# Performance work log

Measured on AMD Instinct MI355X. Metric: run time of the kernel, lower is better.

The kernel has to match this reference:

```python
import jax, jax.numpy as jnp
import numpy as np

B, S, D, H = 2, 4096, 1024, 16
HD = D // H
KCONV = 4


def _rmsnorm(x, scale, eps=1e-6):
    return x * jax.lax.rsqrt(jnp.mean(x * x, axis=-1, keepdims=True) + eps) * scale


def _l2norm(x, eps=1e-6):
    return x * jax.lax.rsqrt(jnp.sum(x * x, axis=-1, keepdims=True) + eps)


def _causal_dwconv_silu(x, w):
    # x: [B,S,D], w: [D,K] depthwise taps (tap K-1 multiplies x[t])
    k = w.shape[1]
    s = x.shape[1]
    xp = jnp.pad(x, ((0, 0), (k - 1, 0), (0, 0)))
    out = sum(xp[:, i:i + s, :] * w[:, i] for i in range(k))
    return jax.nn.silu(out)


def _p20_scan(x, decay_log, theta):
    # BLOCK_DIAGONAL_2 rotary-state linear recurrence: channels paired into
    # complex state, s_t = a * s_{t-1} + u_t with a = exp(-exp(decay_log) + i*theta).
    b, s, d = x.shape
    xc = x.reshape(b, s, d // 2, 2)
    u = jax.lax.complex(xc[..., 0], xc[..., 1])  # [B,S,D/2]
    a = jnp.exp(-jnp.exp(decay_log)) * jnp.exp(1j * theta)  # [D/2] complex, |a|<1

    def step(carry, u_t):
        st = carry * a + u_t
        return st, st

    _, ys = jax.lax.scan(step, jnp.zeros((b, d // 2), u.dtype), jnp.swapaxes(u, 0, 1))
    ys = jnp.swapaxes(ys, 0, 1)  # [B,S,D/2]
    return jnp.stack([ys.real, ys.imag], axis=-1).reshape(b, s, d)


def _gated_delta_rule(q, k, v, g, beta):
    # q,k,v: [B,S,H,Dh]; g,beta: [B,S,H]. State S: [B,H,K,V].
    scale = q.shape[-1] ** -0.5
    q = _l2norm(q)
    k = _l2norm(k)
    qt, kt, vt = (jnp.moveaxis(t, 1, 0) for t in (q, k, v))
    gt, bt = (jnp.moveaxis(t, 1, 0) for t in (g, beta))
    s0 = jnp.zeros((q.shape[0], q.shape[2], q.shape[3], v.shape[3]), v.dtype)

    def step(state, inp):
        q_t, k_t, v_t, g_t, b_t = inp
        state = state * jnp.exp(g_t)[..., None, None]
        v_err = (v_t - jnp.einsum('bhkv,bhk->bhv', state, k_t)) * b_t[..., None]
        state = state + jnp.einsum('bhk,bhv->bhkv', k_t, v_err)
        o_t = jnp.einsum('bhkv,bhk->bhv', state, q_t) * scale
        return state, o_t

    _, o = jax.lax.scan(step, s0, (qt, kt, vt, gt, bt))
    return jnp.moveaxis(o, 0, 1)  # [B,S,H,V]


def setup_inputs() -> dict:
    key = jax.random.key(0)
    ks = jax.random.split(key, 16)
    w = lambda k, shp, s=0.02: (jax.random.normal(k, shp, jnp.float32) * s)
    ctrl_out = 3 * D + 2 * H + D  # q,k,v,decay,beta,output_gate
    ctrl_b = jnp.concatenate([
        jnp.zeros((3 * D,), jnp.float32),
        jnp.full((H,), 1.5, jnp.float32),       # decay bias
        jnp.full((H,), -2.0, jnp.float32),      # beta bias
        jnp.full((D,), -1.5, jnp.float32),      # output gate bias
    ])
    # depthwise conv init: delta at last tap + small noise
    def conv_w(k):
        base = jnp.zeros((D, KCONV), jnp.float32).at[:, -1].set(1.0)
        return base + w(k, (D, KCONV), 0.02)
    return {
        'hidden': jax.random.normal(ks[0], (B, S, D), jnp.float32),
        'p20_decay_log': w(ks[1], (D // 2,), 1.0),
        'p20_theta': jax.random.uniform(ks[2], (D // 2,), jnp.float32, 0.0, 2.0 * np.pi),
        'ctrl_W': w(ks[3], (D, ctrl_out)),
        'ctrl_b': ctrl_b,
        'p20c_W': w(ks[4], (D, 3 * D), 0.001),  # 0.05-scaled init
        'qconv_w': conv_w(ks[5]),
        'kconv_w': conv_w(ks[6]),
        'vconv_w': conv_w(ks[7]),
        'mnorm_scale': jnp.ones((HD,), jnp.float32),
        'vnorm_scale': jnp.ones((D,), jnp.float32),
        'ramp_logit': jnp.full((D,), -4.595, jnp.float32),  # logit(0.01)
        'out_W': w(ks[8], (2 * D, D), 0.02),
        'out_b': jnp.zeros((D,), jnp.float32),
    }


def reference(hidden, p20_decay_log, p20_theta, ctrl_W, ctrl_b, p20c_W,
              qconv_w, kconv_w, vconv_w, mnorm_scale, vnorm_scale,
              ramp_logit, out_W, out_b):
    b, s, d = hidden.shape
    # P20 vector-state side channel
    p20_read = _p20_scan(hidden, p20_decay_log, p20_theta)
    normed_p20 = _rmsnorm(p20_read, vnorm_scale)
    p20_q, p20_k, p20_v = jnp.split(normed_p20 @ p20c_W, 3, axis=-1)
    ramp = jax.nn.sigmoid(ramp_logit)  # [D]
    # packed control projection
    ctrl = hidden @ ctrl_W + ctrl_b
    q_in, k_in, v_in, dec_in, beta_in, gate_in = jnp.split(
        ctrl, np.cumsum([d, d, d, H, H]).tolist(), axis=-1)
    # causal depthwise conv + SiLU
    q_in = _causal_dwconv_silu(q_in, qconv_w)
    k_in = _causal_dwconv_silu(k_in, kconv_w)
    v_in = _causal_dwconv_silu(v_in, vconv_w)
    # P20-conditioned heads
    queries = (q_in + ramp * p20_q).reshape(b, s, H, HD)
    keys = (k_in + ramp * p20_k).reshape(b, s, H, HD)
    values = (v_in + ramp * p20_v).reshape(b, s, H, HD)
    g = jax.nn.log_sigmoid(dec_in.astype(jnp.float32)).astype(hidden.dtype)  # [B,S,H]
    beta = jax.nn.sigmoid(beta_in)
    reads = _gated_delta_rule(queries, keys, values, g, beta)
    normed_reads = _rmsnorm(reads, mnorm_scale).reshape(b, s, d)
    fused = jnp.concatenate([normed_reads, normed_p20], axis=-1)
    projected = fused @ out_W + out_b
    return jax.nn.sigmoid(gate_in) * projected
```

## Files before the change

### kernel.cpp

```cpp
#include <hip/hip_runtime.h>
#include <hip/hip_bf16.h>
#include <stdint.h>

#define SEQ  4096
#define NH   16
#define HD   64

typedef __attribute__((ext_vector_type(8))) short bf16x8;
typedef __attribute__((ext_vector_type(4))) float f32x4;

__device__ __forceinline__ float bf2f(unsigned short u){
  union{unsigned u;float f;} v; v.u = ((unsigned)u)<<16; return v.f;
}
__device__ __forceinline__ unsigned short f2bf(float f){
  union{float f;unsigned u;} v; v.f=f;
  return (unsigned short)((v.u + 0x7fffu + ((v.u>>16)&1u))>>16);
}
__device__ __forceinline__ float sigm(float x){ return 1.f/(1.f+__expf(-x)); }
__device__ __forceinline__ f32x4 mfma16(bf16x8 a, bf16x8 b, f32x4 c){
  return __builtin_amdgcn_mfma_f32_16x16x32_bf16(a,b,c,0,0,0);
}
__device__ __forceinline__ void gll16(const void* g, void* l){
  __builtin_amdgcn_global_load_lds((const __attribute__((address_space(1))) void*)g,
                                   (__attribute__((address_space(3))) void*)l, 16, 0, 0);
}

__global__ void k_fill(float* __restrict__ p, float v, long n){
  long i = (long)blockIdx.x*blockDim.x + threadIdx.x;
  long stride = (long)gridDim.x*blockDim.x;
  for (; i<n; i+=stride) p[i] = v;
}

__global__ void k_cvt_bf16(const float* __restrict__ in, unsigned short* __restrict__ out){
  long i = ((long)blockIdx.x*256 + threadIdx.x)*4;
  float4 v = *(const float4*)(in+i);
  ushort4 o; o.x=f2bf(v.x); o.y=f2bf(v.y); o.z=f2bf(v.z); o.w=f2bf(v.w);
  *(ushort4*)(out+i) = o;
}

__global__ void k_transpose(const float* __restrict__ in, unsigned short* __restrict__ out,
                            int R, int Cin, int Cpad){
  __shared__ float t[32][33];
  int cb = blockIdx.x*32, rb = blockIdx.y*32;
  int tx = threadIdx.x & 31, ty = threadIdx.x >> 5;
  for (int k=0;k<32;k+=8){
    int r = rb+ty+k, c = cb+tx;
    t[ty+k][tx] = (c<Cin) ? in[(long)r*Cin + c] : 0.f;
  }
  __syncthreads();
  for (int k=0;k<32;k+=8){
    int c = cb+ty+k, r = rb+tx;
    if (c<Cpad) out[(long)c*R + r] = f2bf(t[tx][ty+k]);
  }
}

#define FOR16(F) F(0,0) F(0,1) F(0,2) F(0,3) F(1,0) F(1,1) F(1,2) F(1,3) \
                 F(2,0) F(2,1) F(2,2) F(2,3) F(3,0) F(3,1) F(3,2) F(3,3)
#define FOR4(F) F(0) F(1) F(2) F(3)
#define ACC(i,j) Ac##i##j

#define GSTAGE(A_,lda_,Bt_,ldb_,kt_,bs_) do{                                   \
  _Pragma("unroll")                                                            \
  for (int i_=0;i_<2;i_++){                                                    \
    int bo_=i_*4096+wid*1024+l*16;                                             \
    int row_=bo_>>6, ke_=(bo_&63)>>1;                                          \
    gll16((A_)+(m0+row_)*(lda_)+(long)(kt_)*32+ke_, (char*)&Ab[bs_][0]+bo_);   \
    gll16((Bt_)+(n0+row_)*(ldb_)+(long)(kt_)*32+ke_, (char*)&Bb[bs_][0]+bo_);  \
  }}while(0)

#define GEMM_CORE(A_,lda_,Bt_,ldb_,K_)                                         \
  __shared__ unsigned short Ab[2][4096];                                       \
  __shared__ unsigned short Bb[2][4096];                                       \
  const int tid=threadIdx.x, wid=tid>>6, l=tid&63;                             \
  const long m0=(long)blockIdx.y*128, n0=(long)blockIdx.x*128;                 \
  const int nk=(K_)>>5;                                                        \
  const int wm=(wid>>1)*64, wn=(wid&1)*64;                                     \
  f32x4 Ac00={0.f,0.f,0.f,0.f};                                                \
  f32x4 Ac01=Ac00,Ac02=Ac00,Ac03=Ac00,Ac10=Ac00,Ac11=Ac00,Ac12=Ac00,           \
        Ac13=Ac00,Ac20=Ac00,Ac21=Ac00,Ac22=Ac00,Ac23=Ac00,Ac30=Ac00,           \
        Ac31=Ac00,Ac32=Ac00,Ac33=Ac00;                                         \
  GSTAGE(A_,lda_,Bt_,ldb_,0,0);                                                \
  for (int kt=0; kt<nk; ++kt){                                                 \
    __syncthreads();                                                           \
    if (kt+1<nk) GSTAGE(A_,lda_,Bt_,ldb_,kt+1,(kt+1)&1);                       \
    const unsigned short* Apt=&Ab[kt&1][0];                                    \
    const unsigned short* Bpt=&Bb[kt&1][0];                                    \
    const int rao=(wm+(l&15))*32+((l>>4)*8), rbo=(wn+(l&15))*32+((l>>4)*8);    \
    bf16x8 af0=*(const bf16x8*)&Apt[rao];      bf16x8 bf0=*(const bf16x8*)&Bpt[rbo];      \
    bf16x8 af1=*(const bf16x8*)&Apt[rao+512];  bf16x8 bf1=*(const bf16x8*)&Bpt[rbo+512];  \
    bf16x8 af2=*(const bf16x8*)&Apt[rao+1024]; bf16x8 bf2=*(const bf16x8*)&Bpt[rbo+1024]; \
    bf16x8 af3=*(const bf16x8*)&Apt[rao+1536]; bf16x8 bf3=*(const bf16x8*)&Bpt[rbo+1536]; \
    Ac00=mfma16(af0,bf0,Ac00); Ac01=mfma16(af0,bf1,Ac01);                      \
    Ac02=mfma16(af0,bf2,Ac02); Ac03=mfma16(af0,bf3,Ac03);                      \
    Ac10=mfma16(af1,bf0,Ac10); Ac11=mfma16(af1,bf1,Ac11);                      \
    Ac12=mfma16(af1,bf2,Ac12); Ac13=mfma16(af1,bf3,Ac13);                      \
    Ac20=mfma16(af2,bf0,Ac20); Ac21=mfma16(af2,bf1,Ac21);                      \
    Ac22=mfma16(af2,bf2,Ac22); Ac23=mfma16(af2,bf3,Ac23);                      \
    Ac30=mfma16(af3,bf0,Ac30); Ac31=mfma16(af3,bf1,Ac31);                      \
    Ac32=mfma16(af3,bf2,Ac32); Ac33=mfma16(af3,bf3,Ac33);                      \
  }

__global__ __launch_bounds__(256,2) void k_gemm(
  const unsigned short* __restrict__ A, int lda,
  const unsigned short* __restrict__ Bt, int ldb,
  unsigned short* Cb, float* Cf, int ldc,
  int K, int Nvalid,
  const float* __restrict__ bias,
  const unsigned short* __restrict__ gate, int gld)
{
  GEMM_CORE(A, lda, Bt, ldb, K)
#define EPI_GEN(mi,ni) {                                                       \
  const int gn=(int)n0+wn+ni*16+(l&15);                                        \
  if (gn<Nvalid){                                                              \
    _Pragma("unroll") for(int r=0;r<4;r++){                                    \
      const long gm=m0+wm+mi*16+((l>>4)<<2)+r;                                 \
      float v=ACC(mi,ni)[r];                                                   \
      if(bias) v+=bias[gn];                                                    \
      if(gate) v*=bf2f(gate[gm*gld+gn]);                                       \
      if(Cb) Cb[gm*ldc+gn]=f2bf(v); else Cf[gm*ldc+gn]=v; } } }
  FOR16(EPI_GEN)
#undef EPI_GEN
}

__global__ __launch_bounds__(256,2) void k_gemm_ctrl(
  const unsigned short* __restrict__ A, int lda,
  const unsigned short* __restrict__ Bt, int ldb,
  unsigned short* __restrict__ ctrl,
  float* __restrict__ gbuf, float* __restrict__ bbuf,
  unsigned short* __restrict__ gateb,
  const float* __restrict__ bias)
{
  GEMM_CORE(A, lda, Bt, ldb, 1024)
#define EPI_CTRL(mi,ni) {                                                      \
  const int gn=(int)n0+wn+ni*16+(l&15);                                        \
  if (gn<4128){                                                                \
    const float bs=bias[gn];                                                   \
    _Pragma("unroll") for(int r=0;r<4;r++){                                    \
      const long gm=m0+wm+mi*16+((l>>4)<<2)+r;                                 \
      float v=ACC(mi,ni)[r]+bs;                                                \
      if (gn<3072)      ctrl[gm*3072+gn]=f2bf(v);                              \
      else if (gn<3088) gbuf[gm*16+(gn-3072)]=                                 \
                          (v>=0.f)?-log1pf(__expf(-v)):(v-log1pf(__expf(v)));  \
      else if (gn<3104) bbuf[gm*16+(gn-3088)]=sigm(v);                         \
      else              gateb[gm*1024+(gn-3104)]=f2bf(sigm(v)); } } }
  FOR16(EPI_CTRL)
#undef EPI_CTRL
}

__global__ __launch_bounds__(256,2) void k_gemm_qkv(
  const unsigned short* __restrict__ A, int lda,
  const unsigned short* __restrict__ Bt, int ldb,
  const float* __restrict__ ramp,
  unsigned short* __restrict__ Qb, unsigned short* __restrict__ Kb,
  unsigned short* __restrict__ Vb)
{
  GEMM_CORE(A, lda, Bt, ldb, 1024)
  const int seg = (int)((n0 + wn) >> 10);
  unsigned short* Ob = (seg==0)?Qb:((seg==1)?Kb:Vb);
  const int dc0=((int)n0+wn+0*16+(l&15))&1023; const float sr0=sigm(ramp[dc0]);
  const int dc1=((int)n0+wn+1*16+(l&15))&1023; const float sr1=sigm(ramp[dc1]);
  const int dc2=((int)n0+wn+2*16+(l&15))&1023; const float sr2=sigm(ramp[dc2]);
  const int dc3=((int)n0+wn+3*16+(l&15))&1023; const float sr3=sigm(ramp[dc3]);
#define EPI_QKV(mi) {                                                          \
  _Pragma("unroll") for(int r=0;r<4;r++){                                      \
    const long gm=m0+wm+mi*16+((l>>4)<<2)+r;                                   \
    float v0=bf2f(Ob[gm*1024+dc0])+sr0*ACC(mi,0)[r];                           \
    float v1=bf2f(Ob[gm*1024+dc1])+sr1*ACC(mi,1)[r];                           \
    float v2=bf2f(Ob[gm*1024+dc2])+sr2*ACC(mi,2)[r];                           \
    float v3=bf2f(Ob[gm*1024+dc3])+sr3*ACC(mi,3)[r];                           \
    if (seg<2){                                                                \
      float ss=v0*v0+v1*v1+v2*v2+v3*v3;                                        \
      ss+=__shfl_xor(ss,1); ss+=__shfl_xor(ss,2);                              \
      ss+=__shfl_xor(ss,4); ss+=__shfl_xor(ss,8);                              \
      float rs=rsqrtf(ss+1e-6f); v0*=rs; v1*=rs; v2*=rs; v3*=rs; }             \
    Ob[gm*1024+dc0]=f2bf(v0); Ob[gm*1024+dc1]=f2bf(v1);                        \
    Ob[gm*1024+dc2]=f2bf(v2); Ob[gm*1024+dc3]=f2bf(v3); } }
  FOR4(EPI_QKV)
#undef EPI_QKV
}

__global__ void k_scan1(const float* __restrict__ hidden, const float* __restrict__ dlog,
                        const float* __restrict__ theta, float2* __restrict__ finals){
  int idx = blockIdx.x*256 + threadIdx.x;
  int ch = idx & 511; int chunk = (idx>>9) & 63; int b = idx>>15;
  float e = __expf(dlog[ch]); float r = __expf(-e);
  float th = theta[ch]; float ar = r*__cosf(th), ai = r*__sinf(th);
  const float2* src = (const float2*)hidden + ((long)b*SEQ + chunk*64)*512 + ch;
  float sr=0.f, si=0.f;
  for (int j=0;j<64;j++){
    float2 u = src[(long)j*512];
    float nr = sr*ar - si*ai + u.x;
    si = sr*ai + si*ar + u.y; sr = nr;
  }
  finals[idx] = make_float2(sr,si);
}
__global__ void k_scan2(const float* __restrict__ dlog, const float* __restrict__ theta,
                        const float2* __restrict__ finals, float2* __restrict__ carry, int nb){
  int idx = blockIdx.x*256+threadIdx.x; if (idx>=nb*512) return;
  int ch = idx & 511, b = idx>>9;
  float e = __expf(dlog[ch]); float r64 = __expf(-64.f*e);
  float ang = fmodf(64.f*theta[ch], 6.2831853071795864f);
  float cr = r64*__cosf(ang), ci = r64*__sinf(ang);
  float pr=0.f, pi=0.f;
  for (int c=0;c<64;c++){
    long o = ((long)b*64 + c)*512 + ch;
    carry[o] = make_float2(pr,pi);
    float2 f = finals[o];
    float nr = pr*cr - pi*ci + f.x;
    pi = pr*ci + pi*cr + f.y; pr = nr;
  }
}
__global__ void k_scan3(const float* __restrict__ hidden, const float* __restrict__ dlog,
                        const float* __restrict__ theta, const float2* __restrict__ carry,
                        unsigned short* __restrict__ p20){
  int idx = blockIdx.x*256 + threadIdx.x;
  int ch = idx & 511; int chunk = (idx>>9) & 63; int b = idx>>15;
  float e = __expf(dlog[ch]); float r = __expf(-e);
  float th = theta[ch]; float ar = r*__cosf(th), ai = r*__sinf(th);
  long toff = (long)b*SEQ + chunk*64;
  const float2* src = (const float2*)hidden + toff*512 + ch;
  unsigned short* dst = p20 + toff*1024 + 2*ch;
  float2 c0 = carry[idx];
  float sr=c0.x, si=c0.y;
  for (int j=0;j<64;j++){
    float2 u = src[(long)j*512];
    float nr = sr*ar - si*ai + u.x;
    si = sr*ai + si*ar + u.y; sr = nr;
    ushort2 o; o.x=f2bf(sr); o.y=f2bf(si);
    *(ushort2*)(dst + (long)j*1024) = o;
  }
}

__global__ __launch_bounds__(256) void k_rms_p20(const unsigned short* __restrict__ p20,
                        const float* __restrict__ vns, unsigned short* __restrict__ fused){
  long t = blockIdx.x;
  int d = threadIdx.x*4;
  ushort4 xu = *(const ushort4*)(p20 + t*1024 + d);
  float x0=bf2f(xu.x), x1=bf2f(xu.y), x2=bf2f(xu.z), x3=bf2f(xu.w);
  float ss = x0*x0 + x1*x1 + x2*x2 + x3*x3;
  for (int o=1;o<64;o<<=1) ss += __shfl_xor(ss, o);
  __shared__ float red[4];
  if ((threadIdx.x&63)==0) red[threadIdx.x>>6] = ss;
  __syncthreads();
  ss = red[0]+red[1]+red[2]+red[3];
  float rs = rsqrtf(ss*(1.f/1024.f) + 1e-6f);
  float4 s4 = *(const float4*)(vns + d);
  ushort4 o4;
  o4.x = f2bf(x0*rs*s4.x); o4.y = f2bf(x1*rs*s4.y);
  o4.z = f2bf(x2*rs*s4.z); o4.w = f2bf(x3*rs*s4.w);
  *(ushort4*)(fused + t*2048 + 1024 + d) = o4;
}

__global__ __launch_bounds__(256) void k_conv(const unsigned short* __restrict__ ctrl,
   const float* __restrict__ qw, const float* __restrict__ kw, const float* __restrict__ vw,
   unsigned short* __restrict__ Q, unsigned short* __restrict__ Kb, unsigned short* __restrict__ Vb){
  __shared__ unsigned short pan[19][256];
  int panel = blockIdx.x;
  int tb = blockIdx.y;
  int b = tb >> 8; int s0 = (tb & 255) * 16;
  int seg = panel >> 2; int d = (panel & 3)*256 + threadIdx.x;
  int c0 = panel*256;
  long base = (long)b*SEQ*3072;
  for (int rr=0; rr<19; rr++){
    int s = s0 - 3 + rr;
    pan[rr][threadIdx.x] = (s>=0) ? ctrl[base + (long)s*3072 + c0 + threadIdx.x] : (unsigned short)0;
  }
  __syncthreads();
  const float* cw = (seg==0)?qw:((seg==1)?kw:vw);
  float w0=cw[d*4], w1=cw[d*4+1], w2=cw[d*4+2], w3=cw[d*4+3];
  unsigned short* Ob = (seg==0)?Q:((seg==1)?Kb:Vb);
  for (int tk=0; tk<16; tk++){
    long t = (long)b*SEQ + s0 + tk;
    float x = bf2f(pan[tk][threadIdx.x])*w0 + bf2f(pan[tk+1][threadIdx.x])*w1
            + bf2f(pan[tk+2][threadIdx.x])*w2 + bf2f(pan[tk+3][threadIdx.x])*w3;
    x = x * sigm(x);
    Ob[t*1024 + d] = f2bf(x);
  }
}

__global__ __launch_bounds__(64,2) void k_phase1(
    const unsigned short* __restrict__ Kg, const unsigned short* __restrict__ Vg,
    const float* __restrict__ g, const float* __restrict__ beta,
    unsigned short* __restrict__ uvT, unsigned short* __restrict__ Wrm,
    unsigned short* __restrict__ Mc, unsigned short* __restrict__ BcT){
  __shared__ unsigned short Kc[64*64];
  __shared__ unsigned short Vc[64*64];
  __shared__ float Af[64*64];
  __shared__ float uTf[64*69];
  __shared__ float wTf[64*69];
  __shared__ float Gs[64], betl[64], bgam[64], decC[64];

  int bid = blockIdx.x; int bh = bid>>6, c = bid&63;
  int blocal = bh>>4, h = bh&15;
  long t0 = (long)blocal*SEQ + c*64;
  int l = threadIdx.x;
  long cbase = (long)bid*4096;

  float G = g[(t0+l)*16 + h];
  for (int o=1;o<64;o<<=1){ float n = __shfl_up(G,o); if (l>=o) G += n; }
  float bl = beta[(t0+l)*16+h];
  Gs[l]=G; betl[l]=bl; bgam[l]=bl*__expf(G);
  float G63 = __shfl(G,63);
  decC[l] = __expf(G63 - G);
  float GamC = __expf(G63);

  for (int it=0; it<8; it++){
    int bo = it*1024 + l*16;
    int row = bo>>7, bib = bo&127;
    int sb = bib ^ ((row&7)<<4);
    gll16(Kg + (t0+row)*1024 + h*64 + (sb>>1),  (char*)Kc + bo);
    gll16(Vg + (t0+row)*1024 + h*64 + (bib>>1), (char*)Vc + bo);
  }
  __syncthreads();

  bf16x8 kf[2][4];
  {
    int rr = l&15;
    #pragma unroll
    for (int t=0;t<4;t++)
      #pragma unroll
      for (int h2=0;h2<2;h2++){
        int row = t*16 + rr;
        int byt = row*128 + ((h2*64 + (l>>4)*16) ^ ((row&7)<<4));
        kf[h2][t] = *(const bf16x8*)((const char*)Kc + byt);
      }
  }
  #pragma unroll
  for (int ti=0;ti<4;ti++){
    #pragma unroll
    for (int tj=0;tj<4;tj++){
      f32x4 a = {0.f,0.f,0.f,0.f};
      a = mfma16(kf[0][ti], kf[0][tj], a);
      a = mfma16(kf[1][ti], kf[1][tj], a);
      int j = tj*16 + (l&15);
      float Gj = Gs[j];
      #pragma unroll
      for (int r=0;r<4;r++){
        int i = ti*16 + ((l>>4)<<2) + r;
        Af[i*64+j] = (j<i) ? betl[i]*a[r]*__expf(Gs[i]-Gj) : 0.f;
      }
    }
  }
  __syncthreads();

  {
    float uu[64], ww[64];
    #pragma unroll
    for (int i=0;i<64;i++){
      float ua = betl[i]*bf2f(Vc[i*64 + l]);
      float wa = bgam[i]*bf2f(*(const unsigned short*)((const char*)Kc + i*128 + ((2*l) ^ ((i&7)<<4))));
      #pragma unroll
      for (int j=0;j<i;j++){
        float av = Af[i*64+j];
        ua -= av*uu[j];
        wa -= av*ww[j];
      }
      uu[i] = ua; ww[i] = wa;
    }
    #pragma unroll
    for (int i=0;i<64;i++){
      uTf[l*69+i] = uu[i];
      wTf[l*69+i] = ww[i];
    }
  }
  __syncthreads();

  unsigned short* KTp = (unsigned short*)Af;
  for (int j=0;j<64;j++){
    float kv = bf2f(*(const unsigned short*)((const char*)Kc + j*128 + ((2*l) ^ ((j&7)<<4))));
    *(unsigned short*)((char*)KTp + l*128 + ((2*j) ^ ((l&7)<<4))) = f2bf(decC[j]*kv);
  }
  __syncthreads();

  auto ldfragKT = [&](int t, int h2)->bf16x8{
    int row = t*16 + (l&15);
    int byt = row*128 + ((h2*64 + (l>>4)*16) ^ ((row&7)<<4));
    return *(const bf16x8*)((const char*)KTp + byt);
  };
  auto ldfrag69 = [&](const float* base, int nrow, int h2)->bf16x8{
    const float* p = base + nrow*69 + h2*32 + ((l>>4)<<3);
    bf16x8 f;
    #pragma unroll
    for (int q=0;q<8;q++) f[q] = (short)f2bf(p[q]);
    return f;
  };

  #pragma unroll
  for (int to=0; to<4; to++){
    bf16x8 a0 = ldfragKT(to,0), a1 = ldfragKT(to,1);
    #pragma unroll
    for (int tn=0; tn<4; tn++){
      f32x4 accv = {0.f,0.f,0.f,0.f};
      accv = mfma16(a0, ldfrag69(wTf, tn*16+(l&15), 0), accv);
      accv = mfma16(a1, ldfrag69(wTf, tn*16+(l&15), 1), accv);
      int col = tn*16 + (l&15);
      #pragma unroll
      for (int r=0;r<4;r++){
        int row = to*16 + ((l>>4)<<2) + r;
        Mc[cbase + row*64 + col] = f2bf(((row==col)? GamC : 0.f) - accv[r]);
      }
    }
    #pragma unroll
    for (int tv=0; tv<4; tv++){
      f32x4 accv = {0.f,0.f,0.f,0.f};
      accv = mfma16(a0, ldfrag69(uTf, tv*16+(l&15), 0), accv);
      accv = mfma16(a1, ldfrag69(uTf, tv*16+(l&15), 1), accv);
      int v = tv*16 + (l&15);
      int k0 = to*16 + ((l>>4)<<2);
      short4 p;
      p.x=(short)f2bf(accv[0]); p.y=(short)f2bf(accv[1]);
      p.z=(short)f2bf(accv[2]); p.w=(short)f2bf(accv[3]);
      *(short4*)&BcT[cbase + v*64 + k0] = p;
    }
  }

  for (int rr=0; rr<64; rr++){
    uvT[cbase + rr*64 + l] = f2bf(uTf[rr*69 + l]);
    Wrm[cbase + rr*64 + l] = f2bf(wTf[l*69 + rr]);
  }
}

__global__ __launch_bounds__(64,2) void k_phase2(
    const unsigned short* __restrict__ Mc, const unsigned short* __restrict__ BcT,
    unsigned short* __restrict__ Sst){
  __shared__ unsigned short ST[64*64];
  int bh = blockIdx.x; int l = threadIdx.x;
  f32x4 acc[4][4];
  { f32x4 z = {0.f,0.f,0.f,0.f};
    #pragma unroll
    for (int i=0;i<4;i++)
      #pragma unroll
      for (int j=0;j<4;j++) acc[i][j]=z; }

  for (int c=0;c<64;c++){
    long cbase = ((long)bh*64 + c)*4096;
    #pragma unroll
    for (int ti=0;ti<4;ti++){
      #pragma unroll
      for (int tj=0;tj<4;tj++){
        int v = tj*16 + (l&15);
        int kd0 = ti*16 + ((l>>4)<<2);
        short4 p;
        p.x=(short)f2bf(acc[ti][tj][0]); p.y=(short)f2bf(acc[ti][tj][1]);
        p.z=(short)f2bf(acc[ti][tj][2]); p.w=(short)f2bf(acc[ti][tj][3]);
        *(short4*)&Sst[cbase + v*64 + kd0] = p;
        *(short4*)((char*)ST + v*128 + ((2*kd0) ^ ((v&7)<<4))) = p;
      }
    }
    __syncthreads();
    bf16x8 mf[2][4];
    #pragma unroll
    for (int ti=0;ti<4;ti++){
      int row = ti*16 + (l&15);
      mf[0][ti] = *(const bf16x8*)(Mc + cbase + row*64 + (l>>4)*8);
      mf[1][ti] = *(const bf16x8*)(Mc + cbase + row*64 + 32 + (l>>4)*8);
    }
    #pragma unroll
    for (int ti=0;ti<4;ti++)
      #pragma unroll
      for (int tj=0;tj<4;tj++){
        short4 bv = *(const short4*)&BcT[cbase + (long)(tj*16+(l&15))*64 + ti*16 + ((l>>4)<<2)];
        acc[ti][tj][0]=bf2f((unsigned short)bv.x); acc[ti][tj][1]=bf2f((unsigned short)bv.y);
        acc[ti][tj][2]=bf2f((unsigned short)bv.z); acc[ti][tj][3]=bf2f((unsigned short)bv.w);
      }
    bf16x8 sf[2][4];
    #pragma unroll
    for (int tj=0;tj<4;tj++){
      int v = tj*16 + (l&15);
      sf[0][tj] = *(const bf16x8*)((const char*)ST + v*128 + (((l>>4)*16) ^ ((v&7)<<4)));
      sf[1][tj] = *(const bf16x8*)((const char*)ST + v*128 + ((64+(l>>4)*16) ^ ((v&7)<<4)));
    }
    #pragma unroll
    for (int ti=0;ti<4;ti++)
      #pragma unroll
      for (int tj=0;tj<4;tj++){
        acc[ti][tj] = mfma16(mf[0][ti], sf[0][tj], acc[ti][tj]);
        acc[ti][tj] = mfma16(mf[1][ti], sf[1][tj], acc[ti][tj]);
      }
    __syncthreads();
  }
}

__global__ __launch_bounds__(64,2) void k_phase3(
  const unsigned short* __restrict__ Qg, const unsigned short* __restrict__ Kg,
  const float* __restrict__ g,
  const unsigned short* __restrict__ uvT, const unsigned short* __restrict__ Wrm,
  const unsigned short* __restrict__ Sst, const float* __restrict__ mns,
  unsigned short* __restrict__ fused){
  __shared__ unsigned short ST[64*64];
  __shared__ unsigned short QKl[64*64];
  __shared__ unsigned short uT[64*64];
  __shared__ float Gs[64];
  int bid = blockIdx.x; int bh = bid>>6, c = bid&63;
  int blocal = bh>>4, h = bh&15; long t0 = (long)blocal*SEQ + c*64;
  long cbase = (long)bid*4096;
  int l = threadIdx.x;

  float G = g[(t0+l)*16+h];
  for (int o=1;o<64;o<<=1){ float n=__shfl_up(G,o); if(l>=o) G+=n; }
  Gs[l]=G;

  #pragma unroll
  for (int it=0; it<16; it++){
    int flat = it*256 + l*4;
    int v = flat>>6, kd0 = flat&63;
    short4 s4 = *(const short4*)&Sst[cbase + flat];
    *(short4*)((char*)ST + v*128 + ((2*kd0) ^ ((v&7)<<4))) = s4;
  }
  __syncthreads();

  bf16x8 qf[2][4], kfr[2][4], sf[2][4];
  #pragma unroll
  for (int t=0;t<4;t++){
    long tr = t0 + t*16 + (l&15);
    qf[0][t]  = *(const bf16x8*)(Qg + tr*1024 + h*64 + (l>>4)*8);
    qf[1][t]  = *(const bf16x8*)(Qg + tr*1024 + h*64 + 32 + (l>>4)*8);
    kfr[0][t] = *(const bf16x8*)(Kg + tr*1024 + h*64 + (l>>4)*8);
    kfr[1][t] = *(const bf16x8*)(Kg + tr*1024 + h*64 + 32 + (l>>4)*8);
    int v = t*16 + (l&15);
    sf[0][t] = *(const bf16x8*)((const char*)ST + v*128 + (((l>>4)*16) ^ ((v&7)<<4)));
    sf[1][t] = *(const bf16x8*)((const char*)ST + v*128 + ((64+(l>>4)*16) ^ ((v&7)<<4)));
  }

  f32x4 qs[4][4];
  #pragma unroll
  for (int ti=0;ti<4;ti++)
    #pragma unroll
    for (int tj=0;tj<4;tj++){
      f32x4 a = {0.f,0.f,0.f,0.f};
      a = mfma16(qf[0][ti], sf[0][tj], a);
      a = mfma16(qf[1][ti], sf[1][tj], a);
      qs[ti][tj] = a;
    }

  #pragma unroll
  for (int ti=0;ti<4;ti++)
    #pragma unroll
    for (int tj=0;tj<4;tj++){
      f32x4 a = {0.f,0.f,0.f,0.f};
      a = mfma16(qf[0][ti], kfr[0][tj], a);
      a = mfma16(qf[1][ti], kfr[1][tj], a);
      int j = tj*16 + (l&15);
      float Gj = Gs[j];
      #pragma unroll
      for (int r=0;r<4;r++){
        int i = ti*16 + ((l>>4)<<2) + r;
        float v = (j<=i)? a[r]*__expf(Gs[i]-Gj) : 0.f;
        *(unsigned short*)((char*)QKl + i*128 + ((2*j) ^ ((i&7)<<4))) = f2bf(v);
      }
    }

  #pragma unroll
  for (int ti=0; ti<4; ti++){
    int irow = ti*16 + (l&15);
    bf16x8 w0 = *(const bf16x8*)(Wrm + cbase + irow*64 + (l>>4)*8);
    bf16x8 w1 = *(const bf16x8*)(Wrm + cbase + irow*64 + 32 + (l>>4)*8);
    #pragma unroll
    for (int tj=0; tj<4; tj++){
      f32x4 a = {0.f,0.f,0.f,0.f};
      a = mfma16(w0, sf[0][tj], a);
      a = mfma16(w1, sf[1][tj], a);
      int v = tj*16 + (l&15);
      int i0 = ti*16 + ((l>>4)<<2);
      short4 uv4 = *(const short4*)(uvT + cbase + (long)v*64 + i0);
      short4 p;
      p.x=(short)f2bf(bf2f((unsigned short)uv4.x) - a[0]);
      p.y=(short)f2bf(bf2f((unsigned short)uv4.y) - a[1]);
      p.z=(short)f2bf(bf2f((unsigned short)uv4.z) - a[2]);
      p.w=(short)f2bf(bf2f((unsigned short)uv4.w) - a[3]);
      *(short4*)((char*)uT + v*128 + ((2*i0) ^ ((v&7)<<4))) = p;
    }
  }
  __syncthreads();

  float mscale[4];
  #pragma unroll
  for (int tj=0;tj<4;tj++) mscale[tj] = mns[tj*16 + (l&15)];
  #pragma unroll
  for (int ti=0; ti<4; ti++){
    int row = ti*16 + (l&15);
    bf16x8 qk0 = *(const bf16x8*)((const char*)QKl + row*128 + (((l>>4)*16) ^ ((row&7)<<4)));
    bf16x8 qk1 = *(const bf16x8*)((const char*)QKl + row*128 + ((64+(l>>4)*16) ^ ((row&7)<<4)));
    #pragma unroll
    for (int tj=0; tj<4; tj++){
      int v = tj*16 + (l&15);
      bf16x8 u0 = *(const bf16x8*)((const char*)uT + v*128 + (((l>>4)*16) ^ ((v&7)<<4)));
      bf16x8 u1 = *(const bf16x8*)((const char*)uT + v*128 + ((64+(l>>4)*16) ^ ((v&7)<<4)));
      f32x4 a;
      #pragma unroll
      for (int r=0;r<4;r++){
        float gam = __expf(Gs[ti*16 + ((l>>4)<<2) + r]);
        a[r] = qs[ti][tj][r]*gam;
      }
      a = mfma16(qk0,u0,a);
      a = mfma16(qk1,u1,a);
      qs[ti][tj] = a;
    }
  }
  #pragma unroll
  for (int ti=0; ti<4; ti++){
    #pragma unroll
    for (int r=0; r<4; r++){
      float ss = 0.f;
      #pragma unroll
      for (int tj=0;tj<4;tj++){ float v = qs[ti][tj][r]*0.125f; ss += v*v; }
      ss += __shfl_xor(ss,1); ss += __shfl_xor(ss,2); ss += __shfl_xor(ss,4); ss += __shfl_xor(ss,8);
      float rs = rsqrtf(ss*(1.f/64.f) + 1e-6f);
      long t = t0 + ti*16 + ((l>>4)<<2) + r;
      #pragma unroll
      for (int tj=0;tj<4;tj++){
        float on = qs[ti][tj][r]*0.125f*rs*mscale[tj];
        fused[t*2048 + h*64 + tj*16 + (l&15)] = f2bf(on);
      }
    }
  }
}

extern "C" void kernel_launch(void* const* d_in, const int* in_sizes, int n_in,
                              void* d_out, int out_size, void* d_ws, size_t ws_size,
                              hipStream_t stream){
  (void)in_sizes; (void)n_in;
  const float* hidden = (const float*)d_in[0];
  const float* dlog   = (const float*)d_in[1];
  const float* theta  = (const float*)d_in[2];
  const float* ctrlW  = (const float*)d_in[3];
  const float* ctrlb  = (const float*)d_in[4];
  const float* p20cW  = (const float*)d_in[5];
  const float* qw     = (const float*)d_in[6];
  const float* kw     = (const float*)d_in[7];
  const float* vw     = (const float*)d_in[8];
  const float* mns    = (const float*)d_in[9];
  const float* vns    = (const float*)d_in[10];
  const float* ramp   = (const float*)d_in[11];
  const float* outW   = (const float*)d_in[12];
  const float* outb   = (const float*)d_in[13];
  float* out = (float*)d_out;

  struct Bufs {
    unsigned short *ctrl, *uvT, *Wrm, *Mc;
    unsigned short *Qb, *Kb, *Vb, *fused;
    unsigned short *E_hid, *E_p20, *BcT;
    unsigned short *Sst, *gateb, *ctrlWT, *p20WT, *outWT;
    float2 *finals, *carry; float *gbuf, *bbuf;
    size_t need;
  };
  auto mk = [&](size_t NT)->Bufs{
    Bufs B; size_t off=0;
    auto tk=[&](size_t n)->char*{ char* p=(char*)d_ws+off; off += (n+255)&~(size_t)255; return p; };
    char* Rctrl = tk(NT*3072*2);
    B.ctrl=(unsigned short*)Rctrl;
    B.uvT=(unsigned short*)Rctrl; B.Wrm=B.uvT + NT*1024; B.Mc=B.Wrm + NT*1024;
    char* Rqkv = tk(NT*1024*2*3);
    B.Qb=(unsigned short*)Rqkv; B.Kb=B.Qb+NT*1024; B.Vb=B.Kb+NT*1024;
    B.fused=(unsigned short*)tk(NT*2048*2);
    char* RE = tk(NT*1024*2);
    B.E_hid=(unsigned short*)RE; B.E_p20=(unsigned short*)RE; B.BcT=(unsigned short*)RE;
    B.Sst=(unsigned short*)tk(NT*1024*2);
    B.gateb=(unsigned short*)tk(NT*1024*2);
    B.ctrlWT=(unsigned short*)tk((size_t)4224*1024*2);
    B.p20WT=(unsigned short*)tk((size_t)3072*1024*2);
    B.outWT=(unsigned short*)tk((size_t)1024*2048*2);
    B.finals=(float2*)tk(NT*64);
    B.carry=(float2*)tk(NT*64);
    B.gbuf=(float*)tk(NT*16*4);
    B.bbuf=(float*)tk(NT*16*4);
    B.need=off;
    return B;
  };

  Bufs Bf = mk(8192);
  Bufs Bh = mk(4096);
  Bufs B; size_t NT; int nb;
  if      (Bf.need <= ws_size){ B=Bf; NT=8192; nb=2; }
  else if (Bh.need <= ws_size){ B=Bh; NT=4096; nb=1; }
  else {
    k_fill<<<2048,256,0,stream>>>(out, (float)((double)ws_size), (long)out_size);
    return;
  }

  k_transpose<<<dim3(132,32),256,0,stream>>>(ctrlW, B.ctrlWT, 1024, 4128, 4224);
  k_transpose<<<dim3(96,32), 256,0,stream>>>(p20cW, B.p20WT, 1024, 3072, 3072);
  k_transpose<<<dim3(32,64), 256,0,stream>>>(outW,  B.outWT, 2048, 1024, 1024);

  for (int b0=0; b0<2; b0+=nb){
    const float* hidb = hidden + (size_t)b0*SEQ*1024;
    float* outp = out + (size_t)b0*SEQ*1024;
    k_cvt_bf16<<<(int)NT,256,0,stream>>>(hidb, B.E_hid);
    k_gemm_ctrl<<<dim3(33,NT/128),256,0,stream>>>(B.E_hid,1024, B.ctrlWT,1024,
                                                  B.ctrl, B.gbuf, B.bbuf, B.gateb, ctrlb);
    k_scan1<<<nb*128,256,0,stream>>>(hidb,dlog,theta,B.finals);
    k_scan2<<<nb*2, 256,0,stream>>>(dlog,theta,B.finals,B.carry,nb);
    k_scan3<<<nb*128,256,0,stream>>>(hidb,dlog,theta,B.carry,B.E_p20);
    k_rms_p20<<<(int)NT,256,0,stream>>>(B.E_p20,vns,B.fused);
    k_conv<<<dim3(12,NT/16),256,0,stream>>>(B.ctrl,qw,kw,vw,B.Qb,B.Kb,B.Vb);
    k_gemm_qkv<<<dim3(24,NT/128),256,0,stream>>>(B.fused+1024,2048, B.p20WT,1024,
                                                 ramp, B.Qb,B.Kb,B.Vb);
    k_phase1<<<(int)(NT/4),64,0,stream>>>(B.Kb,B.Vb,B.gbuf,B.bbuf,B.uvT,B.Wrm,B.Mc,B.BcT);
    k_phase2<<<nb*16,64,0,stream>>>(B.Mc,B.BcT,B.Sst);
    k_phase3<<<(int)(NT/4),64,0,stream>>>(B.Qb,B.Kb,B.gbuf,B.uvT,B.Wrm,B.Sst,mns,B.fused);
    k_gemm<<<dim3(8,NT/128),256,0,stream>>>(B.fused,2048, B.outWT,2048,
                                            nullptr,outp,1024, 2048,1024, outb, B.gateb,1024);
  }
}
```

Measured before the change: 632.4 us.

## Triple-buffer GEMM LDS staging with XOR swizzle and manual waitcnt

Replaces the double-buffered GEMM k-loop with a three-stage LDS ring, so loads run two iterations ahead. Partial s_waitcnt vmcnt replaces the full wait implied by __syncthreads. Global-to-LDS loads now use an XOR-swizzled chunk layout with matching swizzled fragment reads, aiming to cut LDS bank conflicts. MFMA sections are bracketed with s_setprio. The cost is 50% more LDS per block, which may limit occupancy, and the hand-coded vmcnt accounting is fragile.

```diff
diff --git a/kernel.cpp b/kernel.cpp
--- a/kernel.cpp
+++ b/kernel.cpp
@@ -59,37 +59,53 @@
 #define FOR4(F) F(0) F(1) F(2) F(3)
 #define ACC(i,j) Ac##i##j
 
-#define GSTAGE(A_,lda_,Bt_,ldb_,kt_,bs_) do{                                   \
-  _Pragma("unroll")                                                            \
-  for (int i_=0;i_<2;i_++){                                                    \
-    int bo_=i_*4096+wid*1024+l*16;                                             \
-    int row_=bo_>>6, ke_=(bo_&63)>>1;                                          \
-    gll16((A_)+(m0+row_)*(lda_)+(long)(kt_)*32+ke_, (char*)&Ab[bs_][0]+bo_);   \
-    gll16((Bt_)+(n0+row_)*(ldb_)+(long)(kt_)*32+ke_, (char*)&Bb[bs_][0]+bo_);  \
-  }}while(0)
-
 #define GEMM_CORE(A_,lda_,Bt_,ldb_,K_)                                         \
-  __shared__ unsigned short Ab[2][4096];                                       \
-  __shared__ unsigned short Bb[2][4096];                                       \
+  __shared__ unsigned short Ab[3][4096];                                       \
+  __shared__ unsigned short Bb[3][4096];                                       \
   const int tid=threadIdx.x, wid=tid>>6, l=tid&63;                             \
   const long m0=(long)blockIdx.y*128, n0=(long)blockIdx.x*128;                 \
   const int nk=(K_)>>5;                                                        \
   const int wm=(wid>>1)*64, wn=(wid&1)*64;                                     \
+  const int srow0 = tid>>2;                                                    \
+  const int schunk = (((tid&3) ^ ((tid>>2)&3))<<3);              \
+  const unsigned short* gA0 = (A_) + (m0+srow0)*(lda_) + schunk;               \
+  const unsigned short* gA1 = (A_) + (m0+64+srow0)*(lda_) + schunk;            \
+  const unsigned short* gB0 = (Bt_) + (n0+srow0)*(ldb_) + schunk;              \
+  const unsigned short* gB1 = (Bt_) + (n0+64+srow0)*(ldb_) + schunk;           \
+  const int ldst0 = tid*16, ldst1 = 4096 + tid*16;    \
   f32x4 Ac00={0.f,0.f,0.f,0.f};                                                \
   f32x4 Ac01=Ac00,Ac02=Ac00,Ac03=Ac00,Ac10=Ac00,Ac11=Ac00,Ac12=Ac00,           \
         Ac13=Ac00,Ac20=Ac00,Ac21=Ac00,Ac22=Ac00,Ac23=Ac00,Ac30=Ac00,           \
         Ac31=Ac00,Ac32=Ac00,Ac33=Ac00;                                         \
-  GSTAGE(A_,lda_,Bt_,ldb_,0,0);                                                \
+                                            \
+  gll16(gA0, (char*)&Ab[0][0]+ldst0); gll16(gA1, (char*)&Ab[0][0]+ldst1);      \
+  gll16(gB0, (char*)&Bb[0][0]+ldst0); gll16(gB1, (char*)&Bb[0][0]+ldst1);      \
+  gA0+=32; gA1+=32; gB0+=32; gB1+=32;                                          \
+  gll16(gA0, (char*)&Ab[1][0]+ldst0); gll16(gA1, (char*)&Ab[1][0]+ldst1);      \
+  gll16(gB0, (char*)&Bb[1][0]+ldst0); gll16(gB1, (char*)&Bb[1][0]+ldst1);      \
+  gA0+=32; gA1+=32; gB0+=32; gB1+=32;                                          \
+  int rb=0, sb=2;                                                              \
+  const int sxor = (l&3)<<4;                                                   \
+  const int rao0 = (wm+(l&15))*64 + (((l>>4)<<4) ^ sxor);                      \
+  const int rbo0 = (wn+(l&15))*64 + (((l>>4)<<4) ^ sxor);                      \
   for (int kt=0; kt<nk; ++kt){                                                 \
-    __syncthreads();                                                           \
-    if (kt+1<nk) GSTAGE(A_,lda_,Bt_,ldb_,kt+1,(kt+1)&1);                       \
-    const unsigned short* Apt=&Ab[kt&1][0];                                    \
-    const unsigned short* Bpt=&Bb[kt&1][0];                                    \
-    const int rao=(wm+(l&15))*32+((l>>4)*8), rbo=(wn+(l&15))*32+((l>>4)*8);    \
-    bf16x8 af0=*(const bf16x8*)&Apt[rao];      bf16x8 bf0=*(const bf16x8*)&Bpt[rbo];      \
-    bf16x8 af1=*(const bf16x8*)&Apt[rao+512];  bf16x8 bf1=*(const bf16x8*)&Bpt[rbo+512];  \
-    bf16x8 af2=*(const bf16x8*)&Apt[rao+1024]; bf16x8 bf2=*(const bf16x8*)&Bpt[rbo+1024]; \
-    bf16x8 af3=*(const bf16x8*)&Apt[rao+1536]; bf16x8 bf3=*(const bf16x8*)&Bpt[rbo+1536]; \
+    if (kt+1<nk) { asm volatile("s_waitcnt vmcnt(4)" ::: "memory"); }          \
+    else         { asm volatile("s_waitcnt vmcnt(0)" ::: "memory"); }          \
+    __builtin_amdgcn_sched_barrier(0);                                         \
+    __builtin_amdgcn_s_barrier();                                              \
+    __builtin_amdgcn_sched_barrier(0);                                         \
+    if (kt+2<nk){                                                              \
+      gll16(gA0, (char*)&Ab[sb][0]+ldst0); gll16(gA1, (char*)&Ab[sb][0]+ldst1);\
+      gll16(gB0, (char*)&Bb[sb][0]+ldst0); gll16(gB1, (char*)&Bb[sb][0]+ldst1);\
+      gA0+=32; gA1+=32; gB0+=32; gB1+=32;                                      \
+    }                                                                          \
+    const char* Apt=(const char*)&Ab[rb][0];                                   \
+    const char* Bpt=(const char*)&Bb[rb][0];                                   \
+    bf16x8 af0=*(const bf16x8*)(Apt+rao0);      bf16x8 bf0=*(const bf16x8*)(Bpt+rbo0);      \
+    bf16x8 af1=*(const bf16x8*)(Apt+rao0+1024); bf16x8 bf1=*(const bf16x8*)(Bpt+rbo0+1024); \
+    bf16x8 af2=*(const bf16x8*)(Apt+rao0+2048); bf16x8 bf2=*(const bf16x8*)(Bpt+rbo0+2048); \
+    bf16x8 af3=*(const bf16x8*)(Apt+rao0+3072); bf16x8 bf3=*(const bf16x8*)(Bpt+rbo0+3072); \
+    __builtin_amdgcn_s_setprio(1);                                             \
     Ac00=mfma16(af0,bf0,Ac00); Ac01=mfma16(af0,bf1,Ac01);                      \
     Ac02=mfma16(af0,bf2,Ac02); Ac03=mfma16(af0,bf3,Ac03);                      \
     Ac10=mfma16(af1,bf0,Ac10); Ac11=mfma16(af1,bf1,Ac11);                      \
@@ -98,6 +114,8 @@
     Ac22=mfma16(af2,bf2,Ac22); Ac23=mfma16(af2,bf3,Ac23);                      \
     Ac30=mfma16(af3,bf0,Ac30); Ac31=mfma16(af3,bf1,Ac31);                      \
     Ac32=mfma16(af3,bf2,Ac32); Ac33=mfma16(af3,bf3,Ac33);                      \
+    __builtin_amdgcn_s_setprio(0);                                             \
+    rb = (rb==2)?0:rb+1; sb = (sb==2)?0:sb+1;                                  \
   }
 
 __global__ __launch_bounds__(256,2) void k_gemm(
```

New measurement: 623.8 us. No clear change (-1.4%).
